# Kernel optimization log

Measured on AMD Instinct MI355X. Metric: run time of the kernel, lower is better.

## Reference

```python
import jax, jax.numpy as jnp
import numpy as np

DECAY = 0.99
EPS = 1e-6


def setup_inputs() -> dict:
    key = jax.random.key(0)
    k1, k2, k3, k4 = jax.random.split(key, 4)
    B, L, D, K = 32, 1024, 512, 8192
    return {
        "z_e": jax.random.normal(k1, (B, L, D), dtype=jnp.float32),
        "codebook": jax.random.normal(k2, (K, D), dtype=jnp.float32),
        "cluster_size": jax.random.uniform(k3, (K,), dtype=jnp.float32),
        "ema_w": jax.random.normal(k4, (K, D), dtype=jnp.float32),
    }


def reference(z_e, codebook, cluster_size, ema_w):
    B, L, D = z_e.shape
    K = codebook.shape[0]
    flat = z_e.reshape(-1, D)  # [N, D], N = B*L

    dist = ((flat * flat).sum(1, keepdims=True)
            - 2.0 * flat @ codebook.T
            + (codebook * codebook).sum(1))
    idx = jnp.argmin(dist, axis=1)  # [N]
    z_q = codebook[idx].reshape(B, L, D)

    # EMA statistics (training-mode buffer update); one-hot scatter -> segment_sum
    counts = jax.ops.segment_sum(jnp.ones((B * L,), flat.dtype), idx, num_segments=K)
    dw = jax.ops.segment_sum(flat, idx, num_segments=K)  # [K, D]
    new_cluster_size = DECAY * cluster_size + (1.0 - DECAY) * counts
    new_ema_w = DECAY * ema_w + (1.0 - DECAY) * dw
    n = new_cluster_size.sum()
    cs = (new_cluster_size + EPS) / (n + K * EPS) * n  # Laplace-smoothed counts
    new_codebook = new_ema_w / cs[:, None]

    # loss = mse(sg(z_q), z_e) + 0.25 * mse(z_e, sg(z_q)) = 1.25 * mse
    zq_sg = jax.lax.stop_gradient(z_q)
    loss = 1.25 * jnp.mean((z_e - zq_sg) ** 2)

    # straight-through estimator
    z_q_st = z_e + jax.lax.stop_gradient(z_q - z_e)
    return z_q_st, idx.reshape(B, L), loss, new_codebook, new_cluster_size, new_ema_w
```

## Files before the change

kernel.cpp:

```cpp
#include <hip/hip_runtime.h>


constexpr int N = 32768;
constexpr int D = 512;
constexpr int K = 8192;
constexpr int CAP  = 8192;
constexpr int CAPE = 4096;

constexpr float DECAYF  = 0.99f;
constexpr float OMDECAY = (float)(1.0 - 0.99);
constexpr float EPSF    = 1e-6f;
constexpr float KEPSF   = (float)(8192 * 1e-6);
constexpr float TAU1    = 1.0f;
constexpr float TAU2    = 0.02f;

typedef unsigned int       u32;
typedef unsigned short     u16;
typedef unsigned long long u64;
typedef float  f32x4 __attribute__((ext_vector_type(4)));
typedef u32    u32x4 __attribute__((ext_vector_type(4)));
typedef __bf16 bf16x8 __attribute__((ext_vector_type(8)));

#define AS1 __attribute__((address_space(1)))
#define AS3 __attribute__((address_space(3)))

constexpr size_t OFF_CNORM  = 0;
constexpr size_t OFF_IDX    = OFF_CNORM + K;
constexpr size_t OFF_CNTI   = OFF_IDX + N;
constexpr size_t OFF_FLAGC  = OFF_CNTI + K;
constexpr size_t OFF_FLAG2C = OFF_FLAGC + 1;
constexpr size_t OFF_NEXT   = OFF_FLAG2C + 1;
constexpr size_t OFF_OFFS   = OFF_NEXT + K;
constexpr size_t OFF_LIST   = OFF_OFFS + K + 1;
constexpr size_t OFF_FLAGL  = OFF_LIST + N;
constexpr size_t OFF_FLAG2L = OFF_FLAGL + CAP;
constexpr size_t OFF_PB1    = OFF_FLAG2L + N;
constexpr size_t OFF_PB2    = OFF_PB1 + 16 * CAP;
constexpr size_t OFF_PI1    = OFF_PB2 + 16 * CAP;
constexpr size_t OFF_ESLOT  = (OFF_PI1 + 16 * CAP + 1) & ~(size_t)1;
constexpr size_t OFF_SUMS   = (OFF_ESLOT + 2 * CAPE + 1) & ~(size_t)1;
constexpr size_t OFF_LOSSP  = (OFF_SUMS + 2 + 1) & ~(size_t)1;
constexpr size_t OFF_CBH    = (OFF_LOSSP + 2 * K + 3) & ~(size_t)3;
static_assert((OFF_ESLOT & 1) == 0 && (OFF_SUMS & 1) == 0 && (OFF_LOSSP & 1) == 0, "align");
static_assert((OFF_CBH & 3) == 0, "16B align for global_load_lds");

constexpr size_t OUT_ZQ   = 0;
constexpr size_t OUT_IDX  = OUT_ZQ + (size_t)N * D;
constexpr size_t OUT_LOSS = OUT_IDX + N;
constexpr size_t OUT_NCB  = OUT_LOSS + 1;
constexpr size_t OUT_NCS  = OUT_NCB + (size_t)K * D;
constexpr size_t OUT_EMA  = OUT_NCS + K;
constexpr size_t XH_F  = OUT_ZQ;
constexpr size_t PX2_F = OUT_ZQ + (size_t)N * 256;
constexpr size_t PB1H_F = OUT_EMA;
constexpr size_t PB2H_F = OUT_EMA + 4 * (size_t)N;
constexpr size_t PI1H_F = OUT_EMA + 8 * (size_t)N;

__device__ inline u16 f32_to_bf16_rne(float f)
{
    u32 u = __builtin_bit_cast(u32, f);
    u = (u + 0x7FFFu + ((u >> 16) & 1u)) >> 16;
    return (u16)u;
}

__global__ __launch_bounds__(256) void split_hi_kernel(const float* __restrict__ src,
                                                       u32x4* __restrict__ dst)
{
    const int T = blockIdx.x;
    const int w = threadIdx.x >> 6;
    const int l = threadIdx.x & 63;
    const int row = T * 16 + (l & 15);
#pragma unroll
    for (int i = 0; i < 4; ++i) {
        const int S  = w * 4 + i;
        const int q4 = S * 8 + (l >> 4) * 2;
        const float4 va = ((const float4*)src)[(size_t)row * 128 + q4];
        const float4 vb = ((const float4*)src)[(size_t)row * 128 + q4 + 1];
        const float a[8] = {va.x, va.y, va.z, va.w, vb.x, vb.y, vb.z, vb.w};
        u32x4 o;
#pragma unroll
        for (int j = 0; j < 4; ++j)
            ((u32*)&o)[j] = (u32)f32_to_bf16_rne(a[2 * j]) |
                            ((u32)f32_to_bf16_rne(a[2 * j + 1]) << 16);
        dst[((size_t)T * 16 + S) * 64 + l] = o;
    }
}

__global__ __launch_bounds__(256) void split_int_kernel(const float* __restrict__ src,
                                                        u32x4* __restrict__ dst)
{
    const int R = blockIdx.x;
    const int w = threadIdx.x >> 6;
    const int l = threadIdx.x & 63;
    const int row = R * 16 + (l & 15);
    const int cq  = l >> 4;
#pragma unroll
    for (int i = 0; i < 8; ++i) {
        const int S = w + 4 * i;
        const float4 v = ((const float4*)src)[(size_t)row * 128 + S * 4 + cq];
        u32x4 o;
        const float a[4] = {v.x, v.y, v.z, v.w};
#pragma unroll
        for (int j = 0; j < 4; ++j) {
            const u16 hi = f32_to_bf16_rne(a[j]);
            const float hif = __builtin_bit_cast(float, (u32)hi << 16);
            const u16 lo = f32_to_bf16_rne(a[j] - hif);
            ((u32*)&o)[j] = (u32)hi | ((u32)lo << 16);
        }
        dst[((size_t)R * 32 + S) * 64 + l] = o;
    }
}

__global__ __launch_bounds__(256) void repack_kernel(
    const float* __restrict__ z_e, const int* __restrict__ flag_cnt,
    const int* __restrict__ flag_list, u32x4* __restrict__ PX2)
{
    const int B = blockIdx.x;
    const int cnt = min(*flag_cnt, CAP);
    if (B * 16 >= cnt) return;
    const int w = threadIdx.x >> 6;
    const int l = threadIdx.x & 63;
    const int srow = B * 16 + (l & 15);
    const int n = (srow < cnt) ? (flag_list[srow] & (N - 1)) : 0;
    const int cq = l >> 4;
#pragma unroll
    for (int i = 0; i < 8; ++i) {
        const int S = w + 4 * i;
        const float4 v = ((const float4*)z_e)[(size_t)n * 128 + S * 4 + cq];
        u32x4 o;
        const float a[4] = {v.x, v.y, v.z, v.w};
#pragma unroll
        for (int j = 0; j < 4; ++j) {
            const u16 hi = f32_to_bf16_rne(a[j]);
            const float hif = __builtin_bit_cast(float, (u32)hi << 16);
            const u16 lo = f32_to_bf16_rne(a[j] - hif);
            ((u32*)&o)[j] = (u32)hi | ((u32)lo << 16);
        }
        PX2[((size_t)B * 32 + S) * 64 + l] = o;
    }
}

__global__ __launch_bounds__(256) void row_norm_kernel(const float* __restrict__ a,
                                                       float* __restrict__ out)
{
    const int row  = blockIdx.x * 4 + (threadIdx.x >> 6);
    const int lane = threadIdx.x & 63;
    const float4* r = (const float4*)(a + (size_t)row * D);
    const float4 v0 = r[lane];
    const float4 v1 = r[lane + 64];
    float s = v0.x * v0.x + v0.y * v0.y + v0.z * v0.z + v0.w * v0.w
            + v1.x * v1.x + v1.y * v1.y + v1.z * v1.z + v1.w * v1.w;
#pragma unroll
    for (int m = 32; m >= 1; m >>= 1) s += __shfl_xor(s, m, 64);
    if (lane == 0) out[row] = s;
}

constexpr int BPH = 128, BCH = 512, KIH = 32;
constexpr int NSTEPH = 16;
constexpr int NCHQ   = 4;
constexpr int TOTQ   = NCHQ * NSTEPH;
constexpr int CELH = BCH * KIH;
constexpr int XELH = BPH * KIH;
constexpr int BUFH = CELH + XELH;

__global__ __launch_bounds__(512, 2) void argmin_hi_kernel(
    const u16* __restrict__ CBH, const u16* __restrict__ XH,
    const float* __restrict__ cnorm,
    float* __restrict__ pb1h, float* __restrict__ pb2h, int* __restrict__ pi1h)
{
    __shared__ __align__(16) u16 lds[2][BUFH];

    const int b    = blockIdx.x;
    const int kq   = (b & 7) >> 1;
    const int n0   = ((b >> 3) * 2 + (b & 1)) * BPH;
    const int tid  = threadIdx.x;
    const int w    = tid >> 6;
    const int lane = tid & 63;
    const int lhi  = lane >> 4;

    u32 cbo[4], xo;
#pragma unroll
    for (int m = 0; m < 4; ++m) {
        const int flat = m * 512 + tid;
        cbo[m] = (u32)(kq * 1048576 + (flat >> 6) * 8192 + (flat & 63) * 8);
    }
    xo = (u32)((n0 / 16 + (tid >> 6)) * 8192 + (tid & 63) * 8);

    auto stage = [&](int parity) {
        u16* bufp = &lds[parity][0];
#pragma unroll
        for (int m = 0; m < 4; ++m) {
            __builtin_amdgcn_global_load_lds((const AS1 u32*)(CBH + cbo[m]),
                (AS3 u32*)(bufp + (m * 512 + tid) * 8), 16, 0, 0);
            cbo[m] += 512;
        }
        __builtin_amdgcn_global_load_lds((const AS1 u32*)(XH + xo),
            (AS3 u32*)(bufp + CELH + tid * 8), 16, 0, 0);
        xo += 512;
    };

    float b1[8], b2[8]; int i1[8];
#pragma unroll
    for (int p = 0; p < 8; ++p) { b1[p] = INFINITY; b2[p] = INFINITY; i1[p] = 0; }

    stage(0);
    __syncthreads();
    int sc = 1;

    for (int cc = 0; cc < NCHQ; ++cc) {
        f32x4 acc[4][8];
        const f32x4 zero = {0.f, 0.f, 0.f, 0.f};
#pragma unroll
        for (int cg = 0; cg < 4; ++cg)
#pragma unroll
            for (int p = 0; p < 8; ++p) acc[cg][p] = zero;

        for (int s8 = 0; s8 < NSTEPH; ++s8) {
            const u16* cur = &lds[s8 & 1][0];
            if (sc < TOTQ) {
                if ((sc & (NSTEPH - 1)) == 0) {
#pragma unroll
                    for (int m = 0; m < 4; ++m) cbo[m] += 262144 - 8192;
                    xo -= 8192;
                }
                stage(sc & 1);
                ++sc;
            }
            u32x4 bfr[8];
#pragma unroll
            for (int p = 0; p < 8; ++p)
                bfr[p] = *(const u32x4*)(cur + CELH + p * 512 + lane * 8);
#pragma unroll
            for (int cg = 0; cg < 4; ++cg) {
                const u32x4 af = *(const u32x4*)(cur + (w * 4 + cg) * 512 + lane * 8);
#pragma unroll
                for (int p = 0; p < 8; ++p)
                    acc[cg][p] = __builtin_amdgcn_mfma_f32_16x16x32_bf16(
                        __builtin_bit_cast(bf16x8, af),
                        __builtin_bit_cast(bf16x8, bfr[p]), acc[cg][p], 0, 0, 0);
            }
            __syncthreads();
        }

        const int gchunk = kq * NCHQ + cc;
        const int cb0 = gchunk * BCH + w * 64;
#pragma unroll
        for (int cg = 0; cg < 4; ++cg) {
            const int code0 = cb0 + cg * 16 + lhi * 4;
            const float4 cn4 = *(const float4*)(cnorm + code0);
            const float cn[4] = {cn4.x, cn4.y, cn4.z, cn4.w};
#pragma unroll
            for (int p = 0; p < 8; ++p) {
                const f32x4 A = acc[cg][p];
                const float dv[4] = {cn[0] - 2.f * A.x, cn[1] - 2.f * A.y,
                                     cn[2] - 2.f * A.z, cn[3] - 2.f * A.w};
#pragma unroll
                for (int r = 0; r < 4; ++r) {
                    if (dv[r] < b1[p]) { b2[p] = b1[p]; b1[p] = dv[r]; i1[p] = code0 + r; }
                    else if (dv[r] < b2[p]) { b2[p] = dv[r]; }
                }
            }
        }
    }

#pragma unroll
    for (int p = 0; p < 8; ++p) {
#pragma unroll
        for (int m = 16; m <= 32; m <<= 1) {
            const float ob1 = __shfl_xor(b1[p], m, 64);
            const float ob2 = __shfl_xor(b2[p], m, 64);
            const int   oi1 = __shfl_xor(i1[p], m, 64);
            const float nb2 = fminf(fminf(b2[p], ob2), fmaxf(b1[p], ob1));
            if (ob1 < b1[p] || (ob1 == b1[p] && oi1 < i1[p])) { b1[p] = ob1; i1[p] = oi1; }
            b2[p] = nb2;
        }
    }

    __syncthreads();

    float* mb1 = (float*)&lds[0][0];
    float* mb2 = mb1 + 8 * BPH;
    int*   mi  = (int*)(mb2 + 8 * BPH);
    if (lane < 16) {
#pragma unroll
        for (int p = 0; p < 8; ++p) {
            const int pt = p * 16 + lane;
            mb1[w * BPH + pt] = b1[p];
            mb2[w * BPH + pt] = b2[p];
            mi [w * BPH + pt] = i1[p];
        }
    }
    __syncthreads();
    if (tid < BPH) {
        float fb1 = INFINITY, fb2 = INFINITY; int fi = 0;
        for (int ww = 0; ww < 8; ++ww) {
            const float a1 = mb1[ww * BPH + tid], a2 = mb2[ww * BPH + tid];
            const int   ai = mi[ww * BPH + tid];
            const float nb2 = fminf(fminf(fb2, a2), fmaxf(fb1, a1));
            if (a1 < fb1 || (a1 == fb1 && ai < fi)) { fb1 = a1; fi = ai; }
            fb2 = nb2;
        }
        const int n = n0 + tid;
        pb1h[kq * N + n] = fb1;
        pb2h[kq * N + n] = fb2;
        pi1h[kq * N + n] = fi;
    }
}

__global__ __launch_bounds__(256) void merge_hi_kernel(
    const float* __restrict__ pb1h, const float* __restrict__ pb2h,
    const int* __restrict__ pi1h,
    int* __restrict__ idx_i, float* __restrict__ idx_f,
    int* __restrict__ flag_cnt, int* __restrict__ flag_list,
    int* __restrict__ flag2_cnt, int* __restrict__ flag2_list)
{
    const int n = blockIdx.x * 256 + threadIdx.x;
    float fb1 = INFINITY, fb2 = INFINITY; int fi = 0x7fffffff;
#pragma unroll
    for (int q = 0; q < 4; ++q) {
        const float a1 = pb1h[q * N + n], a2 = pb2h[q * N + n];
        const int   ai = pi1h[q * N + n];
        const float nb2 = fminf(fminf(fb2, a2), fmaxf(fb1, a1));
        if (a1 < fb1 || (a1 == fb1 && ai < fi)) { fb1 = a1; fi = ai; }
        fb2 = nb2;
    }
    idx_i[n] = fi;
    idx_f[n] = (float)fi;
    if (fb2 - fb1 < TAU1) {
        const int pos = atomicAdd(flag_cnt, 1);
        if (pos < CAP) flag_list[pos] = n;
        else {
            const int p2 = atomicAdd(flag2_cnt, 1);
            if ((unsigned)p2 < (unsigned)N) flag2_list[p2] = n;
        }
    }
}

constexpr int CEL2 = 512 * 32;
constexpr int XEL2 = 128 * 32;
constexpr int BUF2 = CEL2 + XEL2;

__global__ __launch_bounds__(512, 2) void argmin_part_kernel(
    const u16* __restrict__ CB2, const u16* __restrict__ PX2,
    const float* __restrict__ cnorm, const int* __restrict__ flag_cnt,
    float* __restrict__ pb1, float* __restrict__ pb2, int* __restrict__ pi1)
{
    const int q  = blockIdx.x & 15;
    const int sb = blockIdx.x >> 4;
    const int cnt = min(*flag_cnt, CAP);
    if (sb * 128 >= cnt) return;
    const int n0s = sb * 128;

    __shared__ __align__(16) u16 lds[2][BUF2];

    const int tid  = threadIdx.x;
    const int w    = tid >> 6;
    const int lane = tid & 63;
    const int lhi  = lane >> 4;

    auto stage = [&](u16* bufp, int s) {
#pragma unroll
        for (int j = 0; j < 4; ++j) {
            const int slot = j * 512 + tid;
            const u16* gsrc = CB2 + (((size_t)(q * 32 + (slot >> 6)) * 32 + s) * 512
                                     + (slot & 63) * 8);
            __builtin_amdgcn_global_load_lds((const AS1 u32*)gsrc,
                                             (AS3 u32*)(bufp + slot * 8), 16, 0, 0);
        }
        const u16* gx = PX2 + (((size_t)(n0s / 16 + (tid >> 6)) * 32 + s) * 512
                               + (tid & 63) * 8);
        __builtin_amdgcn_global_load_lds((const AS1 u32*)gx,
                                         (AS3 u32*)(bufp + CEL2 + tid * 8), 16, 0, 0);
    };

    float b1[8], b2[8]; int i1[8];
#pragma unroll
    for (int p = 0; p < 8; ++p) { b1[p] = INFINITY; b2[p] = INFINITY; i1[p] = 0; }

    f32x4 acc[4][8];
    const f32x4 zero = {0.f, 0.f, 0.f, 0.f};
#pragma unroll
    for (int cg = 0; cg < 4; ++cg)
#pragma unroll
        for (int p = 0; p < 8; ++p) acc[cg][p] = zero;

    stage(&lds[0][0], 0);
    __syncthreads();

#pragma unroll 2
    for (int s = 0; s < 32; ++s) {
        const u16* cur = (s & 1) ? &lds[1][0] : &lds[0][0];
        u16* nxt       = (s & 1) ? &lds[0][0] : &lds[1][0];
        if (s + 1 < 32) stage(nxt, s + 1);

        u32x4 bfr[8];
#pragma unroll
        for (int p = 0; p < 8; ++p)
            bfr[p] = *(const u32x4*)(cur + CEL2 + p * 512 + lane * 8);
#pragma unroll
        for (int cg = 0; cg < 4; ++cg) {
            const u32x4 af = *(const u32x4*)(cur + (w * 4 + cg) * 512 + lane * 8);
            u32x4 as;
            as.x = (af.x >> 16) | (af.x << 16);
            as.y = (af.y >> 16) | (af.y << 16);
            as.z = (af.z >> 16) | (af.z << 16);
            as.w = (af.w >> 16) | (af.w << 16);
#pragma unroll
            for (int p = 0; p < 8; ++p) {
                acc[cg][p] = __builtin_amdgcn_mfma_f32_16x16x32_bf16(
                    __builtin_bit_cast(bf16x8, af), __builtin_bit_cast(bf16x8, bfr[p]),
                    acc[cg][p], 0, 0, 0);
                acc[cg][p] = __builtin_amdgcn_mfma_f32_16x16x32_bf16(
                    __builtin_bit_cast(bf16x8, as), __builtin_bit_cast(bf16x8, bfr[p]),
                    acc[cg][p], 0, 0, 0);
            }
        }
        __syncthreads();
    }

    const int cb0 = q * 512 + w * 64;
#pragma unroll
    for (int cg = 0; cg < 4; ++cg) {
        const int code0 = cb0 + cg * 16 + lhi * 4;
        const float4 cn4 = *(const float4*)(cnorm + code0);
        const float cn[4] = {cn4.x, cn4.y, cn4.z, cn4.w};
#pragma unroll
        for (int p = 0; p < 8; ++p) {
            const f32x4 A = acc[cg][p];
            const float dv[4] = {cn[0] - 2.f * A.x, cn[1] - 2.f * A.y,
                                 cn[2] - 2.f * A.z, cn[3] - 2.f * A.w};
#pragma unroll
            for (int r = 0; r < 4; ++r) {
                if (dv[r] < b1[p]) { b2[p] = b1[p]; b1[p] = dv[r]; i1[p] = code0 + r; }
                else if (dv[r] < b2[p]) { b2[p] = dv[r]; }
            }
        }
    }

#pragma unroll
    for (int p = 0; p < 8; ++p) {
#pragma unroll
        for (int m = 16; m <= 32; m <<= 1) {
            const float ob1 = __shfl_xor(b1[p], m, 64);
            const float ob2 = __shfl_xor(b2[p], m, 64);
            const int   oi1 = __shfl_xor(i1[p], m, 64);
            const float nb2 = fminf(fminf(b2[p], ob2), fmaxf(b1[p], ob1));
            if (ob1 < b1[p] || (ob1 == b1[p] && oi1 < i1[p])) { b1[p] = ob1; i1[p] = oi1; }
            b2[p] = nb2;
        }
    }

    __syncthreads();

    float* mb1 = (float*)&lds[0][0];
    float* mb2 = mb1 + 8 * 128;
    int*   mi  = (int*)(mb2 + 8 * 128);
    if (lane < 16) {
#pragma unroll
        for (int p = 0; p < 8; ++p) {
            const int pt = p * 16 + lane;
            mb1[w * 128 + pt] = b1[p];
            mb2[w * 128 + pt] = b2[p];
            mi [w * 128 + pt] = i1[p];
        }
    }
    __syncthreads();
    if (tid < 128) {
        float fb1 = INFINITY, fb2 = INFINITY; int fi = 0;
        for (int ww = 0; ww < 8; ++ww) {
            const float a1 = mb1[ww * 128 + tid], a2 = mb2[ww * 128 + tid];
            const int   ai = mi[ww * 128 + tid];
            const float nb2 = fminf(fminf(fb2, a2), fmaxf(fb1, a1));
            if (a1 < fb1 || (a1 == fb1 && ai < fi)) { fb1 = a1; fi = ai; }
            fb2 = nb2;
        }
        const int slot = n0s + tid;
        pb1[q * CAP + slot] = fb1;
        pb2[q * CAP + slot] = fb2;
        pi1[q * CAP + slot] = fi;
    }
}

__global__ __launch_bounds__(256) void combine_kernel(
    const int* __restrict__ flag_cnt, const int* __restrict__ flag_list,
    const float* __restrict__ pb1, const float* __restrict__ pb2,
    const int* __restrict__ pi1,
    int* __restrict__ idx_i, float* __restrict__ idx_f,
    int* __restrict__ flag2_cnt, int* __restrict__ flag2_list)
{
    const int s = blockIdx.x * 256 + threadIdx.x;
    const int cnt = min(*flag_cnt, CAP);
    if (s >= cnt) return;
    float fb1 = INFINITY, fb2 = INFINITY; int fi = 0x7fffffff;
#pragma unroll
    for (int q = 0; q < 16; ++q) {
        const float a1 = pb1[q * CAP + s], a2 = pb2[q * CAP + s];
        const int   ai = pi1[q * CAP + s];
        const float nb2 = fminf(fminf(fb2, a2), fmaxf(fb1, a1));
        if (a1 < fb1 || (a1 == fb1 && ai < fi)) { fb1 = a1; fi = ai; }
        fb2 = nb2;
    }
    const int n = flag_list[s] & (N - 1);
    idx_i[n] = fi;
    idx_f[n] = (float)fi;
    if (fb2 - fb1 < TAU2) {
        const int p2 = atomicAdd(flag2_cnt, 1);
        if ((unsigned)p2 < (unsigned)N) flag2_list[p2] = n;
    }
}

__global__ __launch_bounds__(256) void exact_part_kernel(
    const float* __restrict__ x, const float* __restrict__ cb,
    const float* __restrict__ cnorm, const int* __restrict__ flag2_cnt,
    const int* __restrict__ flag2_list, u64* __restrict__ eslot)
{
    __shared__ float4 xs[128];
    __shared__ u64 red[256];
    const int cnt = min(*flag2_cnt, CAPE);
    const int nwork = cnt * 16;
    for (int j = blockIdx.x; j < nwork; j += gridDim.x) {
        const int s = j >> 4;
        const int q = j & 15;
        const int n = flag2_list[s] & (N - 1);
        __syncthreads();
        if (threadIdx.x < 128)
            xs[threadIdx.x] = ((const float4*)(x + (size_t)n * D))[threadIdx.x];
        __syncthreads();
        u64 bestp = ~0ull;
#pragma unroll
        for (int c = 0; c < 2; ++c) {
            const int k = q * 512 + c * 256 + threadIdx.x;
            const float4* crow = (const float4*)(cb + (size_t)k * D);
            float a0 = 0.f, a1 = 0.f, a2 = 0.f, a3 = 0.f;
            for (int d = 0; d < 128; ++d) {
                const float4 xv = xs[d], cv = crow[d];
                a0 = fmaf(xv.x, cv.x, a0);
                a1 = fmaf(xv.y, cv.y, a1);
                a2 = fmaf(xv.z, cv.z, a2);
                a3 = fmaf(xv.w, cv.w, a3);
            }
            const float dist = cnorm[k] - 2.0f * ((a0 + a1) + (a2 + a3));
            u32 ub = __builtin_bit_cast(u32, dist);
            ub = (ub & 0x80000000u) ? ~ub : (ub | 0x80000000u);
            const u64 pk = ((u64)ub << 32) | (u32)k;
            bestp = bestp < pk ? bestp : pk;
        }
        red[threadIdx.x] = bestp;
        __syncthreads();
        for (int off = 128; off > 0; off >>= 1) {
            if (threadIdx.x < off) {
                const u64 o = red[threadIdx.x + off];
                if (o < red[threadIdx.x]) red[threadIdx.x] = o;
            }
            __syncthreads();
        }
        if (threadIdx.x == 0) atomicMin(&eslot[s], red[0]);
    }
}

__global__ __launch_bounds__(256) void exact_write_kernel(
    const int* __restrict__ flag2_cnt, const int* __restrict__ flag2_list,
    const u64* __restrict__ eslot, int* __restrict__ idx_i, float* __restrict__ idx_f)
{
    const int s = blockIdx.x * 256 + threadIdx.x;
    const int cnt = min(*flag2_cnt, CAPE);
    if (s >= cnt) return;
    const int n = flag2_list[s] & (N - 1);
    const int k = (int)(eslot[s] & (u64)(K - 1));
    idx_i[n] = k;
    idx_f[n] = (float)k;
}

__global__ __launch_bounds__(256) void count_kernel(
    const int* __restrict__ idx_i, int* __restrict__ cnti)
{
    const int p = blockIdx.x * 256 + threadIdx.x;
    atomicAdd(&cnti[idx_i[p] & (K - 1)], 1);
}

__global__ __launch_bounds__(256) void scan_kernel(
    const int* __restrict__ cnti, const float* __restrict__ csz,
    int* __restrict__ offs, int* __restrict__ nxt,
    float* __restrict__ ncs, double* __restrict__ n_sum)
{
    __shared__ int    tsum[256];
    __shared__ double dsum[256];
    const int t = threadIdx.x;
    const int base = t * 32;
    int s = 0;
    double dn = 0.0;
#pragma unroll
    for (int i = 0; i < 32; ++i) {
        const int c = cnti[base + i];
        s += c;
        const float v = DECAYF * csz[base + i] + OMDECAY * (float)c;
        ncs[base + i] = v;
        dn += (double)v;
    }
    tsum[t] = s; dsum[t] = dn;
    __syncthreads();
    int run = 0;
    for (int j = 0; j < t; ++j) run += tsum[j];
#pragma unroll
    for (int i = 0; i < 32; ++i) {
        offs[base + i] = run;
        nxt[base + i] = run;
        run += cnti[base + i];
    }
    if (t == 255) offs[K] = run;
    if (t == 0) {
        double tot = 0.0;
        for (int j = 0; j < 256; ++j) tot += dsum[j];
        n_sum[0] = tot;
    }
}

__global__ __launch_bounds__(256) void fill_kernel(
    const int* __restrict__ idx_i, int* __restrict__ nxt, int* __restrict__ list)
{
    const int p = blockIdx.x * 256 + threadIdx.x;
    const int k = idx_i[p] & (K - 1);
    const int pos = atomicAdd(&nxt[k], 1);
    if ((unsigned)pos < (unsigned)N) list[pos] = p;
}

__global__ __launch_bounds__(128) void gather_finalize_kernel(
    const float* __restrict__ x, const float* __restrict__ cb,
    const int* __restrict__ offs, const int* __restrict__ list,
    const float* __restrict__ ema_w, const float* __restrict__ ncs,
    const double* __restrict__ n_sum, float* __restrict__ new_ema,
    float* __restrict__ new_cb, float* __restrict__ zq,
    double* __restrict__ loss_part)
{
    const int k = blockIdx.x;
    const int t = threadIdx.x;
    const int beg = min(offs[k], N), end = min(offs[k + 1], N);
    const size_t o = (size_t)k * 128 + t;
    const float4 c = ((const float4*)cb)[o];
    float4 acc = {0.f, 0.f, 0.f, 0.f};
    float lsum = 0.f;
    for (int i = beg; i < end; ++i) {
        const int p = list[i] & (N - 1);
        const float4 v = ((const float4*)x)[(size_t)p * 128 + t];
        acc.x += v.x; acc.y += v.y; acc.z += v.z; acc.w += v.w;
        ((float4*)zq)[(size_t)p * 128 + t] = c;
        const float d0 = v.x - c.x, d1 = v.y - c.y, d2 = v.z - c.z, d3 = v.w - c.w;
        lsum += d0 * d0 + d1 * d1 + d2 * d2 + d3 * d3;
    }
    const float n = (float)n_sum[0];
    const float csm = (ncs[k] + EPSF) / (n + KEPSF) * n;
    const float4 e = ((const float4*)ema_w)[o];
    float4 ne;
    ne.x = DECAYF * e.x + OMDECAY * acc.x;
    ne.y = DECAYF * e.y + OMDECAY * acc.y;
    ne.z = DECAYF * e.z + OMDECAY * acc.z;
    ne.w = DECAYF * e.w + OMDECAY * acc.w;
    ((float4*)new_ema)[o] = ne;
    float4 nc;
    nc.x = ne.x / csm; nc.y = ne.y / csm; nc.z = ne.z / csm; nc.w = ne.w / csm;
    ((float4*)new_cb)[o] = nc;

#pragma unroll
    for (int m = 32; m >= 1; m >>= 1) lsum += __shfl_xor(lsum, m, 64);
    __shared__ float prt[2];
    if ((t & 63) == 0) prt[t >> 6] = lsum;
    __syncthreads();
    if (t == 0) loss_part[k] = (double)(prt[0] + prt[1]);
}

__global__ __launch_bounds__(256) void loss_reduce_kernel(
    const double* __restrict__ loss_part, float* __restrict__ out_loss)
{
    __shared__ double red[256];
    const int t = threadIdx.x;
    double s = 0.0;
    for (int i = t; i < K; i += 256) s += loss_part[i];
    red[t] = s;
    __syncthreads();
    for (int off = 128; off > 0; off >>= 1) {
        if (t < off) red[t] += red[t + off];
        __syncthreads();
    }
    if (t == 0)
        out_loss[0] = (float)(1.25 * (red[0] / (double)((size_t)N * D)));
}

extern "C" void kernel_launch(void* const* d_in, const int* in_sizes, int n_in,
                              void* d_out, int out_size, void* d_ws, size_t ws_size,
                              hipStream_t stream)
{
    const float* z_e   = (const float*)d_in[0];
    const float* cbook = (const float*)d_in[1];
    const float* csz   = (const float*)d_in[2];
    const float* ema_w = (const float*)d_in[3];

    float* out = (float*)d_out;
    u32*   ws  = (u32*)d_ws;

    float*  cnorm      = (float*)(ws + OFF_CNORM);
    int*    idx_i      = (int*)(ws + OFF_IDX);
    int*    cnti       = (int*)(ws + OFF_CNTI);
    int*    flag_cnt   = (int*)(ws + OFF_FLAGC);
    int*    flag2_cnt  = (int*)(ws + OFF_FLAG2C);
    int*    nxt        = (int*)(ws + OFF_NEXT);
    int*    offs       = (int*)(ws + OFF_OFFS);
    int*    list       = (int*)(ws + OFF_LIST);
    int*    flag_list  = (int*)(ws + OFF_FLAGL);
    int*    flag2_list = (int*)(ws + OFF_FLAG2L);
    float*  pb1        = (float*)(ws + OFF_PB1);
    float*  pb2        = (float*)(ws + OFF_PB2);
    int*    pi1        = (int*)(ws + OFF_PI1);
    u64*    eslot      = (u64*)(ws + OFF_ESLOT);
    double* n_sum      = (double*)(ws + OFF_SUMS);
    double* loss_part  = (double*)(ws + OFF_LOSSP);
    u16*    CBH        = (u16*)(ws + OFF_CBH);

    u16* XH  = (u16*)(out + XH_F);
    u16* PX2 = (u16*)(out + PX2_F);
    u16* CB2 = (u16*)(out + OUT_NCB);
    float* pb1h = out + PB1H_F;
    float* pb2h = out + PB2H_F;
    int*   pi1h = (int*)(out + PI1H_F);

    hipMemsetAsync(ws + OFF_CNTI, 0, (K + 2) * sizeof(u32), stream);
    hipMemsetAsync(ws + OFF_ESLOT, 0xFF, CAPE * sizeof(u64), stream);

    split_hi_kernel<<<N / 16, 256, 0, stream>>>(z_e, (u32x4*)XH);
    split_hi_kernel<<<K / 16, 256, 0, stream>>>(cbook, (u32x4*)CBH);
    split_int_kernel<<<K / 16, 256, 0, stream>>>(cbook, (u32x4*)CB2);
    row_norm_kernel<<<K / 4, 256, 0, stream>>>(cbook, cnorm);

    argmin_hi_kernel<<<(N / BPH) * 4, 512, 0, stream>>>(CBH, XH, cnorm,
                                                        pb1h, pb2h, pi1h);

    merge_hi_kernel<<<N / 256, 256, 0, stream>>>(pb1h, pb2h, pi1h, idx_i,
                                                 out + OUT_IDX, flag_cnt, flag_list,
                                                 flag2_cnt, flag2_list);

    repack_kernel<<<CAP / 16, 256, 0, stream>>>(z_e, flag_cnt, flag_list, (u32x4*)PX2);

    argmin_part_kernel<<<(CAP / 128) * 16, 512, 0, stream>>>(CB2, PX2, cnorm, flag_cnt,
                                                             pb1, pb2, pi1);

    combine_kernel<<<CAP / 256, 256, 0, stream>>>(flag_cnt, flag_list, pb1, pb2, pi1,
                                                  idx_i, out + OUT_IDX,
                                                  flag2_cnt, flag2_list);

    exact_part_kernel<<<2048, 256, 0, stream>>>(z_e, cbook, cnorm, flag2_cnt,
                                                flag2_list, eslot);

    exact_write_kernel<<<CAPE / 256, 256, 0, stream>>>(flag2_cnt, flag2_list, eslot,
                                                       idx_i, out + OUT_IDX);

    count_kernel<<<N / 256, 256, 0, stream>>>(idx_i, cnti);

    scan_kernel<<<1, 256, 0, stream>>>(cnti, csz, offs, nxt, out + OUT_NCS, n_sum);

    fill_kernel<<<N / 256, 256, 0, stream>>>(idx_i, nxt, list);

    gather_finalize_kernel<<<K, 128, 0, stream>>>(z_e, cbook, offs, list, ema_w,
                                                  out + OUT_NCS, n_sum,
                                                  out + OUT_EMA, out + OUT_NCB,
                                                  out + OUT_ZQ, loss_part);

    loss_reduce_kernel<<<1, 256, 0, stream>>>(loss_part, out + OUT_LOSS);
}
```

Measured before the change: 842.5 us.

## Fuse codebook prep kernels and shrink argmin tile to 256 threads

Merges the codebook bf16 split, hi/lo split and row-norm kernels into one cbprep kernel, removing two launches and extra passes over the codebook. It also retiles the high-precision argmin kernel from a 512-code chunk with 8 waves to a 128-code chunk with 4 waves and launch bounds (256,3). Each block now walks 16 chunks instead of 4, which lowers LDS and register use so more blocks can be resident. The cost is that the X tile is reloaded more often relative to codebook data, so reuse per block drops.

```diff
diff --git a/kernel.cpp b/kernel.cpp
--- a/kernel.cpp
+++ b/kernel.cpp
@@ -86,28 +86,61 @@
     }
 }
 
-__global__ __launch_bounds__(256) void split_int_kernel(const float* __restrict__ src,
-                                                        u32x4* __restrict__ dst)
-{
-    const int R = blockIdx.x;
+__global__ __launch_bounds__(256) void cbprep_kernel(const float* __restrict__ cb,
+                                                     u32x4* __restrict__ CBH,
+                                                     u32x4* __restrict__ CB2,
+                                                     float* __restrict__ cnorm)
+{
+    const int T = blockIdx.x;
     const int w = threadIdx.x >> 6;
     const int l = threadIdx.x & 63;
-    const int row = R * 16 + (l & 15);
-    const int cq  = l >> 4;
-#pragma unroll
-    for (int i = 0; i < 8; ++i) {
-        const int S = w + 4 * i;
-        const float4 v = ((const float4*)src)[(size_t)row * 128 + S * 4 + cq];
-        u32x4 o;
-        const float a[4] = {v.x, v.y, v.z, v.w};
-#pragma unroll
-        for (int j = 0; j < 4; ++j) {
-            const u16 hi = f32_to_bf16_rne(a[j]);
-            const float hif = __builtin_bit_cast(float, (u32)hi << 16);
-            const u16 lo = f32_to_bf16_rne(a[j] - hif);
-            ((u32*)&o)[j] = (u32)hi | ((u32)lo << 16);
-        }
-        dst[((size_t)R * 32 + S) * 64 + l] = o;
+    {
+        const int row = T * 16 + (l & 15);
+#pragma unroll
+        for (int i = 0; i < 4; ++i) {
+            const int S  = w * 4 + i;
+            const int q4 = S * 8 + (l >> 4) * 2;
+            const float4 va = ((const float4*)cb)[(size_t)row * 128 + q4];
+            const float4 vb = ((const float4*)cb)[(size_t)row * 128 + q4 + 1];
+            const float a[8] = {va.x, va.y, va.z, va.w, vb.x, vb.y, vb.z, vb.w};
+            u32x4 o;
+#pragma unroll
+            for (int j = 0; j < 4; ++j)
+                ((u32*)&o)[j] = (u32)f32_to_bf16_rne(a[2 * j]) |
+                                ((u32)f32_to_bf16_rne(a[2 * j + 1]) << 16);
+            CBH[((size_t)T * 16 + S) * 64 + l] = o;
+        }
+    }
+    {
+        const int row = T * 16 + (l & 15);
+        const int cq  = l >> 4;
+#pragma unroll
+        for (int i = 0; i < 8; ++i) {
+            const int S = w + 4 * i;
+            const float4 v = ((const float4*)cb)[(size_t)row * 128 + S * 4 + cq];
+            u32x4 o;
+            const float a[4] = {v.x, v.y, v.z, v.w};
+#pragma unroll
+            for (int j = 0; j < 4; ++j) {
+                const u16 hi = f32_to_bf16_rne(a[j]);
+                const float hif = __builtin_bit_cast(float, (u32)hi << 16);
+                const u16 lo = f32_to_bf16_rne(a[j] - hif);
+                ((u32*)&o)[j] = (u32)hi | ((u32)lo << 16);
+            }
+            CB2[((size_t)T * 32 + S) * 64 + l] = o;
+        }
+    }
+#pragma unroll
+    for (int sub = 0; sub < 4; ++sub) {
+        const int row = T * 16 + sub * 4 + w;
+        const float4* r = (const float4*)(cb + (size_t)row * D);
+        const float4 v0 = r[l];
+        const float4 v1 = r[l + 64];
+        float s = v0.x * v0.x + v0.y * v0.y + v0.z * v0.z + v0.w * v0.w
+                + v1.x * v1.x + v1.y * v1.y + v1.z * v1.z + v1.w * v1.w;
+#pragma unroll
+        for (int m = 32; m >= 1; m >>= 1) s += __shfl_xor(s, m, 64);
+        if (l == 0) cnorm[row] = s;
     }
 }
 
@@ -140,30 +173,15 @@
     }
 }
 
-__global__ __launch_bounds__(256) void row_norm_kernel(const float* __restrict__ a,
-                                                       float* __restrict__ out)
-{
-    const int row  = blockIdx.x * 4 + (threadIdx.x >> 6);
-    const int lane = threadIdx.x & 63;
-    const float4* r = (const float4*)(a + (size_t)row * D);
-    const float4 v0 = r[lane];
-    const float4 v1 = r[lane + 64];
-    float s = v0.x * v0.x + v0.y * v0.y + v0.z * v0.z + v0.w * v0.w
-            + v1.x * v1.x + v1.y * v1.y + v1.z * v1.z + v1.w * v1.w;
-#pragma unroll
-    for (int m = 32; m >= 1; m >>= 1) s += __shfl_xor(s, m, 64);
-    if (lane == 0) out[row] = s;
-}
-
-constexpr int BPH = 128, BCH = 512, KIH = 32;
+constexpr int BPH = 128, BCH = 128, KIH = 32;
 constexpr int NSTEPH = 16;
-constexpr int NCHQ   = 4;
+constexpr int NCHQ   = 16;
 constexpr int TOTQ   = NCHQ * NSTEPH;
 constexpr int CELH = BCH * KIH;
 constexpr int XELH = BPH * KIH;
 constexpr int BUFH = CELH + XELH;
 
-__global__ __launch_bounds__(512, 2) void argmin_hi_kernel(
+__global__ __launch_bounds__(256, 3) void argmin_hi_kernel(
     const u16* __restrict__ CBH, const u16* __restrict__ XH,
     const float* __restrict__ cnorm,
     float* __restrict__ pb1h, float* __restrict__ pb2h, int* __restrict__ pi1h)
@@ -178,25 +196,25 @@
     const int lane = tid & 63;
     const int lhi  = lane >> 4;
 
-    u32 cbo[4], xo;
-#pragma unroll
-    for (int m = 0; m < 4; ++m) {
-        const int flat = m * 512 + tid;
+    u32 cbo[2], xo[2];
+#pragma unroll
+    for (int m = 0; m < 2; ++m) {
+        const int flat = m * 256 + tid;
         cbo[m] = (u32)(kq * 1048576 + (flat >> 6) * 8192 + (flat & 63) * 8);
-    }
-    xo = (u32)((n0 / 16 + (tid >> 6)) * 8192 + (tid & 63) * 8);
+        xo[m]  = (u32)((n0 / 16 + (flat >> 6)) * 8192 + (flat & 63) * 8);
+    }
 
     auto stage = [&](int parity) {
         u16* bufp = &lds[parity][0];
 #pragma unroll
-        for (int m = 0; m < 4; ++m) {
+        for (int m = 0; m < 2; ++m) {
             __builtin_amdgcn_global_load_lds((const AS1 u32*)(CBH + cbo[m]),
-                (AS3 u32*)(bufp + (m * 512 + tid) * 8), 16, 0, 0);
+                (AS3 u32*)(bufp + (m * 256 + tid) * 8), 16, 0, 0);
             cbo[m] += 512;
-        }
-        __builtin_amdgcn_global_load_lds((const AS1 u32*)(XH + xo),
-            (AS3 u32*)(bufp + CELH + tid * 8), 16, 0, 0);
-        xo += 512;
+            __builtin_amdgcn_global_load_lds((const AS1 u32*)(XH + xo[m]),
+                (AS3 u32*)(bufp + CELH + (m * 256 + tid) * 8), 16, 0, 0);
+            xo[m] += 512;
+        }
     };
 
     float b1[8], b2[8]; int i1[8];
@@ -208,10 +226,10 @@
     int sc = 1;
 
     for (int cc = 0; cc < NCHQ; ++cc) {
-        f32x4 acc[4][8];
+        f32x4 acc[2][8];
         const f32x4 zero = {0.f, 0.f, 0.f, 0.f};
 #pragma unroll
-        for (int cg = 0; cg < 4; ++cg)
+        for (int cg = 0; cg < 2; ++cg)
 #pragma unroll
             for (int p = 0; p < 8; ++p) acc[cg][p] = zero;
 
@@ -220,8 +238,7 @@
             if (sc < TOTQ) {
                 if ((sc & (NSTEPH - 1)) == 0) {
 #pragma unroll
-                    for (int m = 0; m < 4; ++m) cbo[m] += 262144 - 8192;
-                    xo -= 8192;
+                    for (int m = 0; m < 2; ++m) { cbo[m] += 65536 - 8192; xo[m] -= 8192; }
                 }
                 stage(sc & 1);
                 ++sc;
@@ -231,8 +248,8 @@
             for (int p = 0; p < 8; ++p)
                 bfr[p] = *(const u32x4*)(cur + CELH + p * 512 + lane * 8);
 #pragma unroll
-            for (int cg = 0; cg < 4; ++cg) {
-                const u32x4 af = *(const u32x4*)(cur + (w * 4 + cg) * 512 + lane * 8);
+            for (int cg = 0; cg < 2; ++cg) {
+                const u32x4 af = *(const u32x4*)(cur + (w * 2 + cg) * 512 + lane * 8);
 #pragma unroll
                 for (int p = 0; p < 8; ++p)
                     acc[cg][p] = __builtin_amdgcn_mfma_f32_16x16x32_bf16(
@@ -242,10 +259,9 @@
             __syncthreads();
         }
 
-        const int gchunk = kq * NCHQ + cc;
-        const int cb0 = gchunk * BCH + w * 64;
-#pragma unroll
-        for (int cg = 0; cg < 4; ++cg) {
+        const int cb0 = (kq * NCHQ + cc) * BCH + w * 32;
+#pragma unroll
+        for (int cg = 0; cg < 2; ++cg) {
             const int code0 = cb0 + cg * 16 + lhi * 4;
             const float4 cn4 = *(const float4*)(cnorm + code0);
             const float cn[4] = {cn4.x, cn4.y, cn4.z, cn4.w};
@@ -279,8 +295,8 @@
     __syncthreads();
 
     float* mb1 = (float*)&lds[0][0];
-    float* mb2 = mb1 + 8 * BPH;
-    int*   mi  = (int*)(mb2 + 8 * BPH);
+    float* mb2 = mb1 + 4 * BPH;
+    int*   mi  = (int*)(mb2 + 4 * BPH);
     if (lane < 16) {
 #pragma unroll
         for (int p = 0; p < 8; ++p) {
@@ -293,7 +309,7 @@
     __syncthreads();
     if (tid < BPH) {
         float fb1 = INFINITY, fb2 = INFINITY; int fi = 0;
-        for (int ww = 0; ww < 8; ++ww) {
+        for (int ww = 0; ww < 4; ++ww) {
             const float a1 = mb1[ww * BPH + tid], a2 = mb2[ww * BPH + tid];
             const int   ai = mi[ww * BPH + tid];
             const float nb2 = fminf(fminf(fb2, a2), fmaxf(fb1, a1));
@@ -726,11 +742,9 @@
     hipMemsetAsync(ws + OFF_ESLOT, 0xFF, CAPE * sizeof(u64), stream);
 
     split_hi_kernel<<<N / 16, 256, 0, stream>>>(z_e, (u32x4*)XH);
-    split_hi_kernel<<<K / 16, 256, 0, stream>>>(cbook, (u32x4*)CBH);
-    split_int_kernel<<<K / 16, 256, 0, stream>>>(cbook, (u32x4*)CB2);
-    row_norm_kernel<<<K / 4, 256, 0, stream>>>(cbook, cnorm);
-
-    argmin_hi_kernel<<<(N / BPH) * 4, 512, 0, stream>>>(CBH, XH, cnorm,
+    cbprep_kernel<<<K / 16, 256, 0, stream>>>(cbook, (u32x4*)CBH, (u32x4*)CB2, cnorm);
+
+    argmin_hi_kernel<<<(N / BPH) * 4, 256, 0, stream>>>(CBH, XH, cnorm,
                                                         pb1h, pb2h, pi1h);
 
     merge_hi_kernel<<<N / 256, 256, 0, stream>>>(pb1h, pb2h, pi1h, idx_i,
```

After: 899.4 us. +6.7%, slower.
